# Performance work log

Measured on AMD Instinct MI355X. Metric: run time of the kernel, lower is better.

## Reference

```python
import jax, jax.numpy as jnp
import numpy as np

B, H, W, C = 4, 64, 64, 512
D = C // 8  # query/key channels

def setup_inputs() -> dict:
    key = jax.random.key(0)
    k1, k2, k3, k4, k5 = jax.random.split(key, 5)
    x = jax.random.normal(k1, (B, H, W, C), dtype=jnp.float32)
    # 1x1 convs without bias == per-pixel matmuls; he_normal-ish scaling
    Wq = jax.random.normal(k2, (C, D), dtype=jnp.float32) * np.sqrt(2.0 / C)
    Wk = jax.random.normal(k3, (C, D), dtype=jnp.float32) * np.sqrt(2.0 / C)
    Wv = jax.random.normal(k4, (C, C), dtype=jnp.float32) * np.sqrt(2.0 / C)
    # original init is zeros; use small nonzero so the attention path is exercised
    gamma = jax.random.normal(k5, (1,), dtype=jnp.float32) * 0.1
    return {"x": x, "Wq": Wq, "Wk": Wk, "Wv": Wv, "gamma": gamma}

def reference(x, Wq, Wk, Wv, gamma):
    b, h, w, c = x.shape
    n = h * w
    xf = x.reshape(b, n, c)                      # flatten spatial dims
    q = xf @ Wq                                  # [b, n, c//8]
    k = xf @ Wk                                  # [b, n, c//8]
    v = xf @ Wv                                  # [b, n, c]
    scores = jnp.einsum('bnd,bmd->bnm', q, k)    # [b, n, n]
    attn = jax.nn.sigmoid(scores)                # activation_func='sigmoid' (no row normalization)
    attended = jnp.einsum('bnm,bmc->bnc', attn, v).reshape(b, h, w, c)
    return gamma * attended + x
```

## Files before the change

### kernel.cpp

```cpp
#include <hip/hip_runtime.h>

typedef short bf16x8 __attribute__((ext_vector_type(8)));
typedef float f32x4 __attribute__((ext_vector_type(4)));
typedef unsigned short ushort8v __attribute__((ext_vector_type(8)));
typedef unsigned short ushort4v __attribute__((ext_vector_type(4)));

__device__ __forceinline__ unsigned short f2bf(float f) {
  unsigned u = __float_as_uint(f);
  u += 0x7FFF + ((u >> 16) & 1);
  return (unsigned short)(u >> 16);
}

__global__ void wt_prep(const float* __restrict__ Wq, const float* __restrict__ Wk,
                        const float* __restrict__ Wv, unsigned short* __restrict__ WbT) {
  int idx = blockIdx.x * 256 + threadIdx.x;
  int o = idx >> 9, c = idx & 511;
  float v;
  if (o < 64)       v = Wq[c * 64 + o] * 1.44269504f;
  else if (o < 128) v = Wk[c * 64 + (o - 64)];
  else              v = Wv[(size_t)c * 512 + (o - 128)];
  WbT[idx] = f2bf(v);
}

__global__ __launch_bounds__(256, 2) void proj_gemm(
    const float* __restrict__ x, const unsigned short* __restrict__ WbT,
    unsigned short* __restrict__ q, unsigned short* __restrict__ k,
    unsigned short* __restrict__ vT) {
  __shared__ unsigned short As[128][72];
  const int tid = threadIdx.x;
  const int wid = tid >> 6, lane = tid & 63;
  const int l15 = lane & 15, l4 = lane >> 4;
  const int mtile = blockIdx.x, ntile = blockIdx.y;
  const int rbase = mtile * 128;
  const int wr = (wid >> 1) * 64, wc = (wid & 1) * 64;

  f32x4 acc[4][4] = {};

  const int arow = tid >> 2;
  const int akof = (tid & 3) * 16;

  for (int kb = 0; kb < 512; kb += 64) {
    f32x4 t0[2][4];
#pragma unroll
    for (int pass = 0; pass < 2; ++pass) {
      const float* src = x + (size_t)(rbase + pass * 64 + arow) * 512 + kb + akof;
#pragma unroll
      for (int i = 0; i < 4; ++i) t0[pass][i] = *(const f32x4*)(src + i * 4);
    }
    __syncthreads();
#pragma unroll
    for (int pass = 0; pass < 2; ++pass) {
      unsigned short tmp[16];
#pragma unroll
      for (int i = 0; i < 4; ++i)
#pragma unroll
        for (int j = 0; j < 4; ++j) tmp[i * 4 + j] = f2bf(t0[pass][i][j]);
      unsigned short* dst = &As[pass * 64 + arow][akof];
      *(ushort8v*)(dst)     = *(ushort8v*)(tmp);
      *(ushort8v*)(dst + 8) = *(ushort8v*)(tmp + 8);
    }
    __syncthreads();

    bf16x8 af[4][2], bfr[4][2];
#pragma unroll
    for (int mr = 0; mr < 4; ++mr)
#pragma unroll
      for (int ks = 0; ks < 2; ++ks)
        af[mr][ks] = *(const bf16x8*)&As[wr + mr * 16 + l15][ks * 32 + l4 * 8];
#pragma unroll
    for (int nc = 0; nc < 4; ++nc)
#pragma unroll
      for (int ks = 0; ks < 2; ++ks) {
        int col = ntile * 128 + wc + nc * 16 + l15;
        bfr[nc][ks] = *(const bf16x8*)(WbT + (size_t)col * 512 + kb + ks * 32 + l4 * 8);
      }
#pragma unroll
    for (int ks = 0; ks < 2; ++ks)
#pragma unroll
      for (int mr = 0; mr < 4; ++mr)
#pragma unroll
        for (int nc = 0; nc < 4; ++nc)
          acc[mr][nc] = __builtin_amdgcn_mfma_f32_16x16x32_bf16(af[mr][ks], bfr[nc][ks],
                                                                acc[mr][nc], 0, 0, 0);
  }

  if (ntile == 0) {
    unsigned short* dst = (wid & 1) ? k : q;
#pragma unroll
    for (int mr = 0; mr < 4; ++mr)
#pragma unroll
      for (int nc = 0; nc < 4; ++nc)
#pragma unroll
        for (int r = 0; r < 4; ++r) {
          int grow = rbase + wr + mr * 16 + l4 * 4 + r;
          int col = nc * 16 + l15;
          dst[(size_t)grow * 64 + col] = f2bf(acc[mr][nc][r]);
        }
  } else {
#pragma unroll
    for (int mr = 0; mr < 4; ++mr)
#pragma unroll
      for (int nc = 0; nc < 4; ++nc) {
        int col = ntile * 128 + wc + nc * 16 + l15 - 128;
        int grow = rbase + wr + mr * 16 + l4 * 4;
        int b = grow >> 12, m = grow & 4095;
        ushort4v pk;
#pragma unroll
        for (int r = 0; r < 4; ++r) pk[r] = f2bf(acc[mr][nc][r]);
        *(ushort4v*)(vT + ((size_t)b * 512 + col) * 4096 + m) = pk;
      }
  }
}

__global__ __launch_bounds__(512, 1) void attn_fused(
    const float* __restrict__ x, const unsigned short* __restrict__ q,
    const unsigned short* __restrict__ k, const unsigned short* __restrict__ vT,
    const float* __restrict__ gamma, float* __restrict__ out) {
  __shared__ unsigned short Vs[2][256][72];
  __shared__ unsigned short Ps[2][128][72];
  const int tid = threadIdx.x, w = tid >> 6, lane = tid & 63;
  const int l15 = lane & 15, l4 = lane >> 4;
  const int rhalf = w >> 2;
  const int mt = w & 3;
  const int rt = blockIdx.x, ct = blockIdx.y, b = blockIdx.z;
  const int rbase = rt * 128, cbase = ct * 256;
  const unsigned short* qb = q + (size_t)b * 4096 * 64;
  const unsigned short* kp = k + (size_t)b * 4096 * 64;
  const unsigned short* vb = vT + (size_t)b * 512 * 4096;
  const float gv = gamma[0];

  const int vst_c = tid >> 1, vst_h = (tid & 1) * 32;

  bf16x8 qf[4][2];
#pragma unroll
  for (int rf = 0; rf < 4; ++rf)
#pragma unroll
    for (int ks = 0; ks < 2; ++ks)
      qf[rf][ks] = *(const bf16x8*)(qb +
          (size_t)(rbase + rhalf * 64 + rf * 16 + l15) * 64 + ks * 32 + l4 * 8);

  bf16x8 kfc[2];
#pragma unroll
  for (int ks = 0; ks < 2; ++ks)
    kfc[ks] = *(const bf16x8*)(kp + (size_t)(mt * 16 + l15) * 64 + ks * 32 + l4 * 8);
  {
    bf16x8 vv[4];
#pragma unroll
    for (int i = 0; i < 4; ++i)
      vv[i] = *(const bf16x8*)(vb + (size_t)(cbase + vst_c) * 4096 + vst_h + i * 8);
#pragma unroll
    for (int i = 0; i < 4; ++i) *(bf16x8*)&Vs[0][vst_c][vst_h + i * 8] = vv[i];
  }

  f32x4 oacc[4][4] = {};

  for (int it = 0; it < 64; ++it) {
    const int mb_n = (it + 1) * 64;
    const bool pf = (it < 63);
    const int p = it & 1;
    bf16x8 kfn[2], vv[4];
    if (pf) {
#pragma unroll
      for (int ks = 0; ks < 2; ++ks)
        kfn[ks] = *(const bf16x8*)(kp + (size_t)(mb_n + mt * 16 + l15) * 64 + ks * 32 + l4 * 8);
#pragma unroll
      for (int i = 0; i < 4; ++i)
        vv[i] = *(const bf16x8*)(vb + (size_t)(cbase + vst_c) * 4096 + mb_n + vst_h + i * 8);
    }

    f32x4 sacc[4] = {};
#pragma unroll
    for (int ks = 0; ks < 2; ++ks)
#pragma unroll
      for (int rf = 0; rf < 4; ++rf)
        sacc[rf] = __builtin_amdgcn_mfma_f32_16x16x32_bf16(kfc[ks], qf[rf][ks], sacc[rf], 0, 0, 0);
#pragma unroll
    for (int rf = 0; rf < 4; ++rf) {
      ushort4v pk;
#pragma unroll
      for (int r = 0; r < 4; ++r) {
        float s = sacc[rf][r];
        pk[r] = f2bf(__builtin_amdgcn_rcpf(1.0f + __builtin_amdgcn_exp2f(-s)));
      }
      *(ushort4v*)&Ps[p][rhalf * 64 + rf * 16 + l15][mt * 16 + l4 * 4] = pk;
    }
    __syncthreads();

    __builtin_amdgcn_s_setprio(1);
#pragma unroll
    for (int kk = 0; kk < 2; ++kk) {
      bf16x8 af[4], bfr[4];
#pragma unroll
      for (int mr = 0; mr < 4; ++mr)
        af[mr] = *(const bf16x8*)&Ps[p][rhalf * 64 + mr * 16 + l15][kk * 32 + l4 * 8];
#pragma unroll
      for (int nc = 0; nc < 4; ++nc)
        bfr[nc] = *(const bf16x8*)&Vs[p][mt * 64 + nc * 16 + l15][kk * 32 + l4 * 8];
#pragma unroll
      for (int mr = 0; mr < 4; ++mr)
#pragma unroll
        for (int nc = 0; nc < 4; ++nc)
          oacc[mr][nc] = __builtin_amdgcn_mfma_f32_16x16x32_bf16(af[mr], bfr[nc],
                                                                 oacc[mr][nc], 0, 0, 0);
    }
    __builtin_amdgcn_s_setprio(0);

    if (pf) {
#pragma unroll
      for (int i = 0; i < 4; ++i) *(bf16x8*)&Vs[p ^ 1][vst_c][vst_h + i * 8] = vv[i];
      kfc[0] = kfn[0]; kfc[1] = kfn[1];
    }
  }

#pragma unroll
  for (int mr = 0; mr < 4; ++mr)
#pragma unroll
    for (int nc = 0; nc < 4; ++nc)
#pragma unroll
      for (int r = 0; r < 4; ++r) {
        int grow = rbase + rhalf * 64 + mr * 16 + l4 * 4 + r;
        int col = cbase + mt * 64 + nc * 16 + l15;
        size_t idx = ((size_t)b * 4096 + grow) * 512 + col;
        out[idx] = gv * oacc[mr][nc][r] + x[idx];
      }
}

extern "C" void kernel_launch(void* const* d_in, const int* in_sizes, int n_in,
                              void* d_out, int out_size, void* d_ws, size_t ws_size,
                              hipStream_t stream) {
  const float* x     = (const float*)d_in[0];
  const float* Wq    = (const float*)d_in[1];
  const float* Wk    = (const float*)d_in[2];
  const float* Wv    = (const float*)d_in[3];
  const float* gamma = (const float*)d_in[4];
  float* out = (float*)d_out;

  char* ws = (char*)d_ws;
  unsigned short* qbuf = (unsigned short*)(ws);
  unsigned short* kbuf = (unsigned short*)(ws + (2ull << 20));
  unsigned short* vT   = (unsigned short*)(ws + (4ull << 20));
  unsigned short* WbT  = (unsigned short*)(ws + (20ull << 20));

  hipLaunchKernelGGL(wt_prep, dim3(1280), dim3(256), 0, stream, Wq, Wk, Wv, WbT);
  hipLaunchKernelGGL(proj_gemm, dim3(128, 5), dim3(256), 0, stream, x, WbT, qbuf, kbuf, vT);
  hipLaunchKernelGGL(attn_fused, dim3(32, 2, 4), dim3(512), 0, stream,
                     x, qbuf, kbuf, vT, gamma, out);
}
```

Baseline: 150.6 us.

## Swizzle attention LDS tiles, triple-buffer V, pack bf16 with hardware convert

The padded P and V shared-memory tiles are replaced by unpadded 64-wide rows with an XOR swizzle on 16-byte segments, so the ds reads and writes avoid bank conflicts without padding. V becomes triple-buffered, and the prefetched V tile is now stored before the barrier instead of after the PV MFMAs, which shortens the work done after the matrix ops. Sigmoid outputs are packed two at a time with v_cvt_pk_bf16_f32 in place of the software rounding routine. The extra V buffer raises LDS use. The swizzle indexing adds a little integer arithmetic per access.

```diff
diff --git a/kernel.cpp b/kernel.cpp
--- a/kernel.cpp
+++ b/kernel.cpp
@@ -4,11 +4,18 @@
 typedef float f32x4 __attribute__((ext_vector_type(4)));
 typedef unsigned short ushort8v __attribute__((ext_vector_type(8)));
 typedef unsigned short ushort4v __attribute__((ext_vector_type(4)));
+typedef unsigned int uint2v __attribute__((ext_vector_type(2)));
 
 __device__ __forceinline__ unsigned short f2bf(float f) {
   unsigned u = __float_as_uint(f);
   u += 0x7FFF + ((u >> 16) & 1);
   return (unsigned short)(u >> 16);
+}
+
+__device__ __forceinline__ unsigned cvt_pk_bf16(float lo, float hi) {
+  unsigned r;
+  asm("v_cvt_pk_bf16_f32 %0, %1, %2" : "=v"(r) : "v"(lo), "v"(hi));
+  return r;
 }
 
 __global__ void wt_prep(const float* __restrict__ Wq, const float* __restrict__ Wk,
@@ -116,8 +123,8 @@
     const float* __restrict__ x, const unsigned short* __restrict__ q,
     const unsigned short* __restrict__ k, const unsigned short* __restrict__ vT,
     const float* __restrict__ gamma, float* __restrict__ out) {
-  __shared__ unsigned short Vs[2][256][72];
-  __shared__ unsigned short Ps[2][128][72];
+  __shared__ unsigned short Vs[3][256 * 64];
+  __shared__ unsigned short Ps[2][128 * 64];
   const int tid = threadIdx.x, w = tid >> 6, lane = tid & 63;
   const int l15 = lane & 15, l4 = lane >> 4;
   const int rhalf = w >> 2;
@@ -129,7 +136,7 @@
   const unsigned short* vb = vT + (size_t)b * 512 * 4096;
   const float gv = gamma[0];
 
-  const int vst_c = tid >> 1, vst_h = (tid & 1) * 32;
+  const int vst_c = tid >> 1, vst_x = tid & 1;
 
   bf16x8 qf[4][2];
 #pragma unroll
@@ -147,17 +154,20 @@
     bf16x8 vv[4];
 #pragma unroll
     for (int i = 0; i < 4; ++i)
-      vv[i] = *(const bf16x8*)(vb + (size_t)(cbase + vst_c) * 4096 + vst_h + i * 8);
-#pragma unroll
-    for (int i = 0; i < 4; ++i) *(bf16x8*)&Vs[0][vst_c][vst_h + i * 8] = vv[i];
+      vv[i] = *(const bf16x8*)(vb + (size_t)(cbase + vst_c) * 4096 + vst_x * 32 + i * 8);
+#pragma unroll
+    for (int i = 0; i < 4; ++i)
+      *(bf16x8*)&Vs[0][vst_c * 64 + ((vst_x * 4 + i) ^ (vst_c & 7)) * 8] = vv[i];
   }
 
   f32x4 oacc[4][4] = {};
+  int cur = 0;
 
   for (int it = 0; it < 64; ++it) {
     const int mb_n = (it + 1) * 64;
     const bool pf = (it < 63);
     const int p = it & 1;
+    int wbuf = cur + 1; if (wbuf == 3) wbuf = 0;
     bf16x8 kfn[2], vv[4];
     if (pf) {
 #pragma unroll
@@ -165,7 +175,7 @@
         kfn[ks] = *(const bf16x8*)(kp + (size_t)(mb_n + mt * 16 + l15) * 64 + ks * 32 + l4 * 8);
 #pragma unroll
       for (int i = 0; i < 4; ++i)
-        vv[i] = *(const bf16x8*)(vb + (size_t)(cbase + vst_c) * 4096 + mb_n + vst_h + i * 8);
+        vv[i] = *(const bf16x8*)(vb + (size_t)(cbase + vst_c) * 4096 + mb_n + vst_x * 32 + i * 8);
     }
 
     f32x4 sacc[4] = {};
@@ -174,15 +184,26 @@
 #pragma unroll
       for (int rf = 0; rf < 4; ++rf)
         sacc[rf] = __builtin_amdgcn_mfma_f32_16x16x32_bf16(kfc[ks], qf[rf][ks], sacc[rf], 0, 0, 0);
+
 #pragma unroll
     for (int rf = 0; rf < 4; ++rf) {
-      ushort4v pk;
-#pragma unroll
-      for (int r = 0; r < 4; ++r) {
-        float s = sacc[rf][r];
-        pk[r] = f2bf(__builtin_amdgcn_rcpf(1.0f + __builtin_amdgcn_exp2f(-s)));
-      }
-      *(ushort4v*)&Ps[p][rhalf * 64 + rf * 16 + l15][mt * 16 + l4 * 4] = pk;
+      float pv[4];
+#pragma unroll
+      for (int r = 0; r < 4; ++r)
+        pv[r] = __builtin_amdgcn_rcpf(1.0f + __builtin_amdgcn_exp2f(-sacc[rf][r]));
+      uint2v pk;
+      pk[0] = cvt_pk_bf16(pv[0], pv[1]);
+      pk[1] = cvt_pk_bf16(pv[2], pv[3]);
+      int row = rhalf * 64 + rf * 16 + l15;
+      int seg = 2 * mt + (l4 >> 1);
+      *(uint2v*)&Ps[p][row * 64 + ((seg ^ (row & 7)) << 3) + (l4 & 1) * 4] = pk;
+    }
+
+    if (pf) {
+#pragma unroll
+      for (int i = 0; i < 4; ++i)
+        *(bf16x8*)&Vs[wbuf][vst_c * 64 + ((vst_x * 4 + i) ^ (vst_c & 7)) * 8] = vv[i];
+      kfc[0] = kfn[0]; kfc[1] = kfn[1];
     }
     __syncthreads();
 
@@ -191,11 +212,15 @@
     for (int kk = 0; kk < 2; ++kk) {
       bf16x8 af[4], bfr[4];
 #pragma unroll
-      for (int mr = 0; mr < 4; ++mr)
-        af[mr] = *(const bf16x8*)&Ps[p][rhalf * 64 + mr * 16 + l15][kk * 32 + l4 * 8];
-#pragma unroll
-      for (int nc = 0; nc < 4; ++nc)
-        bfr[nc] = *(const bf16x8*)&Vs[p][mt * 64 + nc * 16 + l15][kk * 32 + l4 * 8];
+      for (int mr = 0; mr < 4; ++mr) {
+        int row = rhalf * 64 + mr * 16 + l15;
+        af[mr] = *(const bf16x8*)&Ps[p][row * 64 + (((kk * 4 + l4) ^ (row & 7)) << 3)];
+      }
+#pragma unroll
+      for (int nc = 0; nc < 4; ++nc) {
+        int rowv = mt * 64 + nc * 16 + l15;
+        bfr[nc] = *(const bf16x8*)&Vs[cur][rowv * 64 + (((kk * 4 + l4) ^ (rowv & 7)) << 3)];
+      }
 #pragma unroll
       for (int mr = 0; mr < 4; ++mr)
 #pragma unroll
@@ -204,12 +229,7 @@
                                                                  oacc[mr][nc], 0, 0, 0);
     }
     __builtin_amdgcn_s_setprio(0);
-
-    if (pf) {
-#pragma unroll
-      for (int i = 0; i < 4; ++i) *(bf16x8*)&Vs[p ^ 1][vst_c][vst_h + i * 8] = vv[i];
-      kfc[0] = kfn[0]; kfc[1] = kfn[1];
-    }
+    cur = wbuf;
   }
 
 #pragma unroll
```

Measured after the change: 161.3 us. 1.07x slower.

## Split-K the P·V MFMA across wave pairs with an LDS reduction epilogue

Applied to the files above, without the earlier changes.

The P·V product is repartitioned. Each wave now covers all 128 query rows and one 64-column slice of V, but only half of the 64-key chunk, instead of a 64-row by 64-column tile over the full chunk. This cuts the shared-memory fragment loads per wave per iteration (12 instead of 16) while keeping the MFMA count the same. The cost is a doubled accumulator register footprint and a new epilogue. In that epilogue, partial sums from the odd waves go through LDS, reusing the V buffer, and are added by the even waves, with extra barriers.

```diff
diff --git a/kernel.cpp b/kernel.cpp
--- a/kernel.cpp
+++ b/kernel.cpp
@@ -122,13 +122,14 @@
   const int l15 = lane & 15, l4 = lane >> 4;
   const int rhalf = w >> 2;
   const int mt = w & 3;
+  const int pvt = w >> 1;
+  const int ms = w & 1;
   const int rt = blockIdx.x, ct = blockIdx.y, b = blockIdx.z;
   const int rbase = rt * 128, cbase = ct * 256;
   const unsigned short* qb = q + (size_t)b * 4096 * 64;
   const unsigned short* kp = k + (size_t)b * 4096 * 64;
   const unsigned short* vb = vT + (size_t)b * 512 * 4096;
   const float gv = gamma[0];
-
   const int vst_c = tid >> 1, vst_h = (tid & 1) * 32;
 
   bf16x8 qf[4][2];
@@ -152,7 +153,7 @@
     for (int i = 0; i < 4; ++i) *(bf16x8*)&Vs[0][vst_c][vst_h + i * 8] = vv[i];
   }
 
-  f32x4 oacc[4][4] = {};
+  f32x4 oacc[8][4] = {};
 
   for (int it = 0; it < 64; ++it) {
     const int mb_n = (it + 1) * 64;
@@ -174,6 +175,7 @@
 #pragma unroll
       for (int rf = 0; rf < 4; ++rf)
         sacc[rf] = __builtin_amdgcn_mfma_f32_16x16x32_bf16(kfc[ks], qf[rf][ks], sacc[rf], 0, 0, 0);
+
 #pragma unroll
     for (int rf = 0; rf < 4; ++rf) {
       ushort4v pk;
@@ -187,17 +189,16 @@
     __syncthreads();
 
     __builtin_amdgcn_s_setprio(1);
-#pragma unroll
-    for (int kk = 0; kk < 2; ++kk) {
-      bf16x8 af[4], bfr[4];
-#pragma unroll
-      for (int mr = 0; mr < 4; ++mr)
-        af[mr] = *(const bf16x8*)&Ps[p][rhalf * 64 + mr * 16 + l15][kk * 32 + l4 * 8];
+    {
+      bf16x8 af[8], bfr[4];
+#pragma unroll
+      for (int mr = 0; mr < 8; ++mr)
+        af[mr] = *(const bf16x8*)&Ps[p][mr * 16 + l15][ms * 32 + l4 * 8];
 #pragma unroll
       for (int nc = 0; nc < 4; ++nc)
-        bfr[nc] = *(const bf16x8*)&Vs[p][mt * 64 + nc * 16 + l15][kk * 32 + l4 * 8];
-#pragma unroll
-      for (int mr = 0; mr < 4; ++mr)
+        bfr[nc] = *(const bf16x8*)&Vs[p][pvt * 64 + nc * 16 + l15][ms * 32 + l4 * 8];
+#pragma unroll
+      for (int mr = 0; mr < 8; ++mr)
 #pragma unroll
         for (int nc = 0; nc < 4; ++nc)
           oacc[mr][nc] = __builtin_amdgcn_mfma_f32_16x16x32_bf16(af[mr], bfr[nc],
@@ -207,22 +208,45 @@
 
     if (pf) {
 #pragma unroll
-      for (int i = 0; i < 4; ++i) *(bf16x8*)&Vs[p ^ 1][vst_c][vst_h + i * 8] = vv[i];
+      for (int i = 0; i < 4; ++i)
+        *(bf16x8*)&Vs[p ^ 1][vst_c][vst_h + i * 8] = vv[i];
       kfc[0] = kfn[0]; kfc[1] = kfn[1];
     }
   }
 
-#pragma unroll
-  for (int mr = 0; mr < 4; ++mr)
-#pragma unroll
-    for (int nc = 0; nc < 4; ++nc)
-#pragma unroll
-      for (int r = 0; r < 4; ++r) {
-        int grow = rbase + rhalf * 64 + mr * 16 + l4 * 4 + r;
-        int col = cbase + mt * 64 + nc * 16 + l15;
-        size_t idx = ((size_t)b * 4096 + grow) * 512 + col;
-        out[idx] = gv * oacc[mr][nc][r] + x[idx];
-      }
+  float* red = (float*)&Vs[0][0][0];
+  __syncthreads();
+#pragma unroll
+  for (int h = 0; h < 2; ++h) {
+    if (ms == 1) {
+#pragma unroll
+      for (int m4 = 0; m4 < 4; ++m4)
+#pragma unroll
+        for (int nc = 0; nc < 4; ++nc)
+#pragma unroll
+          for (int r = 0; r < 4; ++r)
+            red[((pvt * 64 + m4 * 16 + l4 * 4 + r)) * 68 + nc * 16 + l15 +
+                (size_t)0] = oacc[h * 4 + m4][nc][r];
+    }
+    __syncthreads();
+    if (ms == 0) {
+#pragma unroll
+      for (int m4 = 0; m4 < 4; ++m4)
+#pragma unroll
+        for (int nc = 0; nc < 4; ++nc)
+#pragma unroll
+          for (int r = 0; r < 4; ++r) {
+            int mr = h * 4 + m4;
+            float sum = oacc[mr][nc][r] +
+                red[((pvt * 64 + m4 * 16 + l4 * 4 + r)) * 68 + nc * 16 + l15];
+            int grow = rbase + mr * 16 + l4 * 4 + r;
+            int col = cbase + pvt * 64 + nc * 16 + l15;
+            size_t idx = ((size_t)b * 4096 + grow) * 512 + col;
+            out[idx] = gv * sum + x[idx];
+          }
+    }
+    __syncthreads();
+  }
 }
 
 extern "C" void kernel_launch(void* const* d_in, const int* in_sizes, int n_in,
```

New measurement: 144.2 us. -4.3%, faster.

## Retile attention: 64-row blocks over all channels, load V straight into registers

Applied to the files above, without the earlier changes.

The attention kernel now gives each block 64 query rows and all 512 output channels, with each of the 8 waves owning 64 channels. This replaces the old 128-row by 256-channel tiles. V fragments are loaded from global memory directly into registers with a one-step register prefetch, so the V shared-memory buffer and its stores go away. The aim is to cut LDS traffic and avoid recomputing scores twice per row block. In exchange, every wave reads its own V slice from global memory each step, V is reread for every 64 rows instead of every 128, and register pressure rises.

```diff
diff --git a/kernel.cpp b/kernel.cpp
--- a/kernel.cpp
+++ b/kernel.cpp
@@ -116,41 +116,36 @@
     const float* __restrict__ x, const unsigned short* __restrict__ q,
     const unsigned short* __restrict__ k, const unsigned short* __restrict__ vT,
     const float* __restrict__ gamma, float* __restrict__ out) {
-  __shared__ unsigned short Vs[2][256][72];
-  __shared__ unsigned short Ps[2][128][72];
+  __shared__ unsigned short Ps[2][64][72];
   const int tid = threadIdx.x, w = tid >> 6, lane = tid & 63;
   const int l15 = lane & 15, l4 = lane >> 4;
-  const int rhalf = w >> 2;
+  const int qp = w >> 2;
   const int mt = w & 3;
-  const int rt = blockIdx.x, ct = blockIdx.y, b = blockIdx.z;
-  const int rbase = rt * 128, cbase = ct * 256;
+  const int rt = blockIdx.x, b = blockIdx.y;
+  const int rbase = rt * 64;
   const unsigned short* qb = q + (size_t)b * 4096 * 64;
   const unsigned short* kp = k + (size_t)b * 4096 * 64;
   const unsigned short* vb = vT + (size_t)b * 512 * 4096;
   const float gv = gamma[0];
 
-  const int vst_c = tid >> 1, vst_h = (tid & 1) * 32;
-
-  bf16x8 qf[4][2];
-#pragma unroll
-  for (int rf = 0; rf < 4; ++rf)
+  bf16x8 qf[2][2];
+#pragma unroll
+  for (int j = 0; j < 2; ++j)
 #pragma unroll
     for (int ks = 0; ks < 2; ++ks)
-      qf[rf][ks] = *(const bf16x8*)(qb +
-          (size_t)(rbase + rhalf * 64 + rf * 16 + l15) * 64 + ks * 32 + l4 * 8);
-
-  bf16x8 kfc[2];
+      qf[j][ks] = *(const bf16x8*)(qb +
+          (size_t)(rbase + (qp * 2 + j) * 16 + l15) * 64 + ks * 32 + l4 * 8);
+
+  bf16x8 kfc[2], kfn[2], vC[8], vN[8];
 #pragma unroll
   for (int ks = 0; ks < 2; ++ks)
     kfc[ks] = *(const bf16x8*)(kp + (size_t)(mt * 16 + l15) * 64 + ks * 32 + l4 * 8);
-  {
-    bf16x8 vv[4];
-#pragma unroll
-    for (int i = 0; i < 4; ++i)
-      vv[i] = *(const bf16x8*)(vb + (size_t)(cbase + vst_c) * 4096 + vst_h + i * 8);
-#pragma unroll
-    for (int i = 0; i < 4; ++i) *(bf16x8*)&Vs[0][vst_c][vst_h + i * 8] = vv[i];
-  }
+#pragma unroll
+  for (int nc = 0; nc < 4; ++nc)
+#pragma unroll
+    for (int kk = 0; kk < 2; ++kk)
+      vC[nc * 2 + kk] = *(const bf16x8*)(vb +
+          (size_t)(w * 64 + nc * 16 + l15) * 4096 + kk * 32 + l4 * 8);
 
   f32x4 oacc[4][4] = {};
 
@@ -158,57 +153,57 @@
     const int mb_n = (it + 1) * 64;
     const bool pf = (it < 63);
     const int p = it & 1;
-    bf16x8 kfn[2], vv[4];
     if (pf) {
 #pragma unroll
       for (int ks = 0; ks < 2; ++ks)
         kfn[ks] = *(const bf16x8*)(kp + (size_t)(mb_n + mt * 16 + l15) * 64 + ks * 32 + l4 * 8);
 #pragma unroll
-      for (int i = 0; i < 4; ++i)
-        vv[i] = *(const bf16x8*)(vb + (size_t)(cbase + vst_c) * 4096 + mb_n + vst_h + i * 8);
-    }
-
-    f32x4 sacc[4] = {};
+      for (int nc = 0; nc < 4; ++nc)
+#pragma unroll
+        for (int kk = 0; kk < 2; ++kk)
+          vN[nc * 2 + kk] = *(const bf16x8*)(vb +
+              (size_t)(w * 64 + nc * 16 + l15) * 4096 + mb_n + kk * 32 + l4 * 8);
+    }
+
+    f32x4 sacc[2] = {};
 #pragma unroll
     for (int ks = 0; ks < 2; ++ks)
 #pragma unroll
-      for (int rf = 0; rf < 4; ++rf)
-        sacc[rf] = __builtin_amdgcn_mfma_f32_16x16x32_bf16(kfc[ks], qf[rf][ks], sacc[rf], 0, 0, 0);
-#pragma unroll
-    for (int rf = 0; rf < 4; ++rf) {
+      for (int j = 0; j < 2; ++j)
+        sacc[j] = __builtin_amdgcn_mfma_f32_16x16x32_bf16(kfc[ks], qf[j][ks], sacc[j], 0, 0, 0);
+
+#pragma unroll
+    for (int j = 0; j < 2; ++j) {
       ushort4v pk;
 #pragma unroll
       for (int r = 0; r < 4; ++r) {
-        float s = sacc[rf][r];
+        float s = sacc[j][r];
         pk[r] = f2bf(__builtin_amdgcn_rcpf(1.0f + __builtin_amdgcn_exp2f(-s)));
       }
-      *(ushort4v*)&Ps[p][rhalf * 64 + rf * 16 + l15][mt * 16 + l4 * 4] = pk;
+      *(ushort4v*)&Ps[p][(qp * 2 + j) * 16 + l15][mt * 16 + l4 * 4] = pk;
     }
     __syncthreads();
 
     __builtin_amdgcn_s_setprio(1);
 #pragma unroll
     for (int kk = 0; kk < 2; ++kk) {
-      bf16x8 af[4], bfr[4];
+      bf16x8 af[4];
 #pragma unroll
       for (int mr = 0; mr < 4; ++mr)
-        af[mr] = *(const bf16x8*)&Ps[p][rhalf * 64 + mr * 16 + l15][kk * 32 + l4 * 8];
-#pragma unroll
-      for (int nc = 0; nc < 4; ++nc)
-        bfr[nc] = *(const bf16x8*)&Vs[p][mt * 64 + nc * 16 + l15][kk * 32 + l4 * 8];
+        af[mr] = *(const bf16x8*)&Ps[p][mr * 16 + l15][kk * 32 + l4 * 8];
 #pragma unroll
       for (int mr = 0; mr < 4; ++mr)
 #pragma unroll
         for (int nc = 0; nc < 4; ++nc)
-          oacc[mr][nc] = __builtin_amdgcn_mfma_f32_16x16x32_bf16(af[mr], bfr[nc],
+          oacc[mr][nc] = __builtin_amdgcn_mfma_f32_16x16x32_bf16(af[mr], vC[nc * 2 + kk],
                                                                  oacc[mr][nc], 0, 0, 0);
     }
     __builtin_amdgcn_s_setprio(0);
 
     if (pf) {
-#pragma unroll
-      for (int i = 0; i < 4; ++i) *(bf16x8*)&Vs[p ^ 1][vst_c][vst_h + i * 8] = vv[i];
       kfc[0] = kfn[0]; kfc[1] = kfn[1];
+#pragma unroll
+      for (int i = 0; i < 8; ++i) vC[i] = vN[i];
     }
   }
 
@@ -218,8 +213,8 @@
     for (int nc = 0; nc < 4; ++nc)
 #pragma unroll
       for (int r = 0; r < 4; ++r) {
-        int grow = rbase + rhalf * 64 + mr * 16 + l4 * 4 + r;
-        int col = cbase + mt * 64 + nc * 16 + l15;
+        int grow = rbase + mr * 16 + l4 * 4 + r;
+        int col = w * 64 + nc * 16 + l15;
         size_t idx = ((size_t)b * 4096 + grow) * 512 + col;
         out[idx] = gv * oacc[mr][nc][r] + x[idx];
       }
@@ -243,6 +238,6 @@
 
   hipLaunchKernelGGL(wt_prep, dim3(1280), dim3(256), 0, stream, Wq, Wk, Wv, WbT);
   hipLaunchKernelGGL(proj_gemm, dim3(128, 5), dim3(256), 0, stream, x, WbT, qbuf, kbuf, vT);
-  hipLaunchKernelGGL(attn_fused, dim3(32, 2, 4), dim3(512), 0, stream,
+  hipLaunchKernelGGL(attn_fused, dim3(64, 4), dim3(512), 0, stream,
                      x, qbuf, kbuf, vT, gamma, out);
 }
```

Result: slower. 201.5 us (+33.8%).
